# Optimization experiments

Measured on AMD Instinct MI355X. Metric: run time of the kernel, lower is better.

The kernel has to match this reference:

```python
import jax, jax.numpy as jnp
import numpy as np

DIM = 1024
N_HEADS = 16
HEAD_DIM = DIM // N_HEADS


def setup_inputs() -> dict:
    key = jax.random.key(0)
    k1, k2, k3 = jax.random.split(key, 3)
    x = jax.random.normal(k1, (1, 4096, DIM), dtype=jnp.float32)
    # nn.Linear weights stored as [out, in]; y = x @ W.T
    w_qkv = jax.random.normal(k2, (3 * DIM, DIM), dtype=jnp.float32) * (DIM ** -0.5)
    w_o = jax.random.normal(k3, (DIM, DIM), dtype=jnp.float32) * (DIM ** -0.5)
    return {"x": x, "w_qkv": w_qkv, "w_o": w_o}


def reference(x, w_qkv, w_o):
    b, s, _ = x.shape
    qkv = jnp.einsum('bsd,ed->bse', x, w_qkv)  # [b, s, 3*dim]
    qkv = qkv.reshape(b, s, 3, N_HEADS, HEAD_DIM)
    qkv = jnp.transpose(qkv, (2, 0, 3, 1, 4))  # [3, b, h, s, hd]
    q, k, v = qkv[0], qkv[1], qkv[2]
    scale = HEAD_DIM ** -0.5
    scores = jnp.einsum('bhqd,bhkd->bhqk', q, k) * scale  # full O(N^2) scores
    attn = jax.nn.softmax(scores, axis=-1)
    out = jnp.einsum('bhqk,bhkd->bhqd', attn, v)
    out = jnp.transpose(out, (0, 2, 1, 3)).reshape(b, s, DIM)
    return jnp.einsum('bsd,ed->bse', out, w_o)
```

## Files before the change

### kernel.cpp

```cpp
#include <hip/hip_runtime.h>

typedef __bf16 bf16x8 __attribute__((ext_vector_type(8)));
typedef float f32x4 __attribute__((ext_vector_type(4)));
typedef unsigned short ushort_t;
typedef unsigned int uint_t;

constexpr int S = 4096, DMODEL = 1024, NH = 16, HD = 64;
#define QSCALE 0.18033688011112042f

#if __has_builtin(__builtin_amdgcn_exp2f)
#define EXP2(x) __builtin_amdgcn_exp2f(x)
#else
#define EXP2(x) exp2f(x)
#endif

__device__ inline ushort_t f2bf(float f) {
  uint_t u = __builtin_bit_cast(uint_t, f);
  u = u + 0x7FFFu + ((u >> 16) & 1u);
  return (ushort_t)(u >> 16);
}

__device__ inline ushort_t f2bf_hw(float f) {
  __bf16 h = (__bf16)f;
  return __builtin_bit_cast(ushort_t, h);
}

__device__ inline void gl2lds16(const ushort_t* g, ushort_t* l) {
  __builtin_amdgcn_global_load_lds(
      (const __attribute__((address_space(1))) unsigned int*)g,
      (__attribute__((address_space(3))) unsigned int*)l, 16, 0, 0);
}

__global__ __launch_bounds__(256) void cvt_f32_bf16(const float* __restrict__ in,
                                                    ushort_t* __restrict__ out, int n4) {
  int i = blockIdx.x * 256 + threadIdx.x;
  if (i >= n4) return;
  float4 f = reinterpret_cast<const float4*>(in)[i];
  ushort4 o;
  o.x = f2bf(f.x); o.y = f2bf(f.y); o.z = f2bf(f.z); o.w = f2bf(f.w);
  reinterpret_cast<ushort4*>(out)[i] = o;
}

template <int EPI>
__global__ __launch_bounds__(256) void gemm_bt(const ushort_t* __restrict__ A,
                                               const ushort_t* __restrict__ B,
                                               int M, int N, int K,
                                               float* __restrict__ Cf,
                                               ushort_t* __restrict__ qb,
                                               ushort_t* __restrict__ kb,
                                               ushort_t* __restrict__ vtb) {
  __shared__ ushort_t sA[128 * 64];
  __shared__ ushort_t sB[128 * 64];
  const int t = threadIdx.x;
  const int lane = t & 63, w = t >> 6;
  const int wr = w >> 1, wc = w & 1;
  const int rA0 = blockIdx.y * 128, rB0 = blockIdx.x * 128;

  f32x4 acc[4][4];
#pragma unroll
  for (int m = 0; m < 4; ++m)
#pragma unroll
    for (int n = 0; n < 4; ++n) acc[m][n] = (f32x4){0.f, 0.f, 0.f, 0.f};

  const int srow = t >> 3;
  const int scol = (t & 7) * 8;
  const int ldsbase = w * 512;

  for (int k0 = 0; k0 < K; k0 += 64) {
#pragma unroll
    for (int i = 0; i < 4; ++i) {
      int r = i * 32 + srow;
      int kc = scol ^ ((r & 7) << 3);
      gl2lds16(&A[(size_t)(rA0 + r) * K + k0 + kc], &sA[i * 2048 + ldsbase]);
    }
#pragma unroll
    for (int i = 0; i < 4; ++i) {
      int r = i * 32 + srow;
      int kc = scol ^ ((r & 7) << 3);
      gl2lds16(&B[(size_t)(rB0 + r) * K + k0 + kc], &sB[i * 2048 + ldsbase]);
    }
    __syncthreads();
#pragma unroll
    for (int ks = 0; ks < 2; ++ks) {
      const int kk = ks * 32 + (lane >> 4) * 8;
      bf16x8 af[4], bfr[4];
#pragma unroll
      for (int m = 0; m < 4; ++m) {
        int row = wr * 64 + m * 16 + (lane & 15);
        af[m] = *(const bf16x8*)&sA[row * 64 + (kk ^ ((row & 7) << 3))];
      }
#pragma unroll
      for (int n = 0; n < 4; ++n) {
        int row = wc * 64 + n * 16 + (lane & 15);
        bfr[n] = *(const bf16x8*)&sB[row * 64 + (kk ^ ((row & 7) << 3))];
      }
#pragma unroll
      for (int m = 0; m < 4; ++m)
#pragma unroll
        for (int n = 0; n < 4; ++n)
          acc[m][n] = __builtin_amdgcn_mfma_f32_16x16x32_bf16(af[m], bfr[n], acc[m][n], 0, 0, 0);
    }
    __syncthreads();
  }

#pragma unroll
  for (int m = 0; m < 4; ++m)
#pragma unroll
    for (int n = 0; n < 4; ++n)
#pragma unroll
      for (int r = 0; r < 4; ++r) {
        int row = rA0 + wr * 64 + m * 16 + (lane >> 4) * 4 + r;
        int col = rB0 + wc * 64 + n * 16 + (lane & 15);
        float v = acc[m][n][r];
        if constexpr (EPI == 0) {
          Cf[(size_t)row * N + col] = v;
        } else {
          int t3 = col >> 10, h = (col >> 6) & 15, d = col & 63;
          if (t3 == 0)      qb[((size_t)h * S + row) * HD + d] = f2bf_hw(v * QSCALE);
          else if (t3 == 1) kb[((size_t)h * S + row) * HD + d] = f2bf_hw(v);
          else              vtb[((size_t)h * HD + d) * S + row] = f2bf_hw(v);
        }
      }
}

__global__ __launch_bounds__(256) void gemm_bt_n64(const ushort_t* __restrict__ A,
                                                   const ushort_t* __restrict__ B,
                                                   int M, int N, int K,
                                                   float* __restrict__ Cf) {
  __shared__ ushort_t sA[128 * 64];
  __shared__ ushort_t sB[64 * 64];
  const int t = threadIdx.x;
  const int lane = t & 63, w = t >> 6;
  const int wr = w >> 1, wc = w & 1;
  const int rA0 = blockIdx.y * 128, rB0 = blockIdx.x * 64;

  f32x4 acc[4][2];
#pragma unroll
  for (int m = 0; m < 4; ++m)
#pragma unroll
    for (int n = 0; n < 2; ++n) acc[m][n] = (f32x4){0.f, 0.f, 0.f, 0.f};

  const int srow = t >> 3;
  const int scol = (t & 7) * 8;
  const int ldsbase = w * 512;

  for (int k0 = 0; k0 < K; k0 += 64) {
#pragma unroll
    for (int i = 0; i < 4; ++i) {
      int r = i * 32 + srow;
      int kc = scol ^ ((r & 7) << 3);
      gl2lds16(&A[(size_t)(rA0 + r) * K + k0 + kc], &sA[i * 2048 + ldsbase]);
    }
#pragma unroll
    for (int i = 0; i < 2; ++i) {
      int r = i * 32 + srow;
      int kc = scol ^ ((r & 7) << 3);
      gl2lds16(&B[(size_t)(rB0 + r) * K + k0 + kc], &sB[i * 2048 + ldsbase]);
    }
    __syncthreads();
#pragma unroll
    for (int ks = 0; ks < 2; ++ks) {
      const int kk = ks * 32 + (lane >> 4) * 8;
      bf16x8 af[4], bfr[2];
#pragma unroll
      for (int m = 0; m < 4; ++m) {
        int row = wr * 64 + m * 16 + (lane & 15);
        af[m] = *(const bf16x8*)&sA[row * 64 + (kk ^ ((row & 7) << 3))];
      }
#pragma unroll
      for (int n = 0; n < 2; ++n) {
        int row = wc * 32 + n * 16 + (lane & 15);
        bfr[n] = *(const bf16x8*)&sB[row * 64 + (kk ^ ((row & 7) << 3))];
      }
#pragma unroll
      for (int m = 0; m < 4; ++m)
#pragma unroll
        for (int n = 0; n < 2; ++n)
          acc[m][n] = __builtin_amdgcn_mfma_f32_16x16x32_bf16(af[m], bfr[n], acc[m][n], 0, 0, 0);
    }
    __syncthreads();
  }

#pragma unroll
  for (int m = 0; m < 4; ++m)
#pragma unroll
    for (int n = 0; n < 2; ++n)
#pragma unroll
      for (int r = 0; r < 4; ++r) {
        int row = rA0 + wr * 64 + m * 16 + (lane >> 4) * 4 + r;
        int col = rB0 + wc * 32 + n * 16 + (lane & 15);
        Cf[(size_t)row * N + col] = acc[m][n][r];
      }
}

__global__ __launch_bounds__(512) void attn_fwd(const ushort_t* __restrict__ qb,
                                                const ushort_t* __restrict__ kb,
                                                const ushort_t* __restrict__ vtb,
                                                ushort_t* __restrict__ aob) {
  __shared__ ushort_t sK[3][64 * 64];
  __shared__ ushort_t sV[3][64 * 64];
  __shared__ ushort_t sP[8][16 * 64];
  const int t = threadIdx.x, lane = t & 63, w = t >> 6;
  const int f = blockIdx.x;
  const int sidx = (f & 7) * 64 + (f >> 3);
  const int h = sidx >> 5;
  const int q0 = (sidx & 31) * 128;
  const ushort_t* qh = qb + (size_t)h * S * HD;
  const ushort_t* kh = kb + (size_t)h * S * HD;
  const ushort_t* vh = vtb + (size_t)h * HD * S;

  bf16x8 qf[2];
  {
    int qr = q0 + w * 16 + (lane & 15);
    const ushort_t* p = &qh[(size_t)qr * HD + (lane >> 4) * 8];
    qf[0] = *(const bf16x8*)p;
    qf[1] = *(const bf16x8*)(p + 32);
  }
  f32x4 acc[4];
#pragma unroll
  for (int n = 0; n < 4; ++n) acc[n] = (f32x4){0.f, 0.f, 0.f, 0.f};
  float lsum[4] = {0.f, 0.f, 0.f, 0.f};

  const int srow = t >> 3;
  const int scol = (t & 7) * 8;
  const int kc = scol ^ ((srow & 7) << 3);
  const int ldsbase = w * 512;
  const int kk0 = (lane >> 4) * 8;

  auto stage = [&](int buf, int kv0) {
    gl2lds16(&kh[(size_t)(kv0 + srow) * HD + kc], &sK[buf][ldsbase]);
    gl2lds16(&vh[(size_t)srow * S + kv0 + kc], &sV[buf][ldsbase]);
  };

  constexpr int NT = S / 64;
  stage(0, 0);
  stage(1, 64);

  for (int ti = 0; ti < NT; ++ti) {
    const int buf = ti % 3;
    if (ti + 2 < NT) {
      stage((ti + 2) % 3, (ti + 2) * 64);
      asm volatile("s_waitcnt vmcnt(4)" ::: "memory");
    } else if (ti + 1 < NT) {
      asm volatile("s_waitcnt vmcnt(2)" ::: "memory");
    } else {
      asm volatile("s_waitcnt vmcnt(0)" ::: "memory");
    }
    __builtin_amdgcn_sched_barrier(0);
    __builtin_amdgcn_s_barrier();

    const ushort_t* Kb = &sK[buf][0];
    const ushort_t* Vb = &sV[buf][0];

    f32x4 sc[4];
    __builtin_amdgcn_s_setprio(1);
#pragma unroll
    for (int nt = 0; nt < 4; ++nt) {
      sc[nt] = (f32x4){0.f, 0.f, 0.f, 0.f};
      int row = nt * 16 + (lane & 15);
#pragma unroll
      for (int ks = 0; ks < 2; ++ks) {
        int kk = ks * 32 + kk0;
        bf16x8 kf = *(const bf16x8*)&Kb[row * 64 + (kk ^ ((row & 7) << 3))];
        sc[nt] = __builtin_amdgcn_mfma_f32_16x16x32_bf16(qf[ks], kf, sc[nt], 0, 0, 0);
      }
    }
    __builtin_amdgcn_s_setprio(0);

    float p[4][4];
#pragma unroll
    for (int r = 0; r < 4; ++r) {
      float ps = 0.f;
#pragma unroll
      for (int nt = 0; nt < 4; ++nt) {
        float pv = EXP2(sc[nt][r]);
        p[nt][r] = pv;
        ps += pv;
      }
      lsum[r] += ps;
    }
    const int prow_base = (lane >> 4) * 4;
#pragma unroll
    for (int nt = 0; nt < 4; ++nt) {
      int col = nt * 16 + (lane & 15);
#pragma unroll
      for (int r = 0; r < 4; ++r) {
        int row = prow_base + r;
        sP[w][row * 64 + (col ^ ((row & 7) << 3))] = f2bf_hw(p[nt][r]);
      }
    }
    bf16x8 pf[2];
    {
      int row = lane & 15;
#pragma unroll
      for (int ks = 0; ks < 2; ++ks) {
        int kk = ks * 32 + kk0;
        pf[ks] = *(const bf16x8*)&sP[w][row * 64 + (kk ^ ((row & 7) << 3))];
      }
    }
    __builtin_amdgcn_s_setprio(1);
#pragma unroll
    for (int nt = 0; nt < 4; ++nt) {
      int row = nt * 16 + (lane & 15);
#pragma unroll
      for (int ks = 0; ks < 2; ++ks) {
        int kk = ks * 32 + kk0;
        bf16x8 vf = *(const bf16x8*)&Vb[row * 64 + (kk ^ ((row & 7) << 3))];
        acc[nt] = __builtin_amdgcn_mfma_f32_16x16x32_bf16(pf[ks], vf, acc[nt], 0, 0, 0);
      }
    }
    __builtin_amdgcn_s_setprio(0);
    __builtin_amdgcn_s_barrier();
  }
  float linv[4];
#pragma unroll
  for (int r = 0; r < 4; ++r) {
    float l = lsum[r];
    l += __shfl_xor(l, 1);
    l += __shfl_xor(l, 2);
    l += __shfl_xor(l, 4);
    l += __shfl_xor(l, 8);
    linv[r] = 1.0f / l;
  }
#pragma unroll
  for (int nt = 0; nt < 4; ++nt)
#pragma unroll
    for (int r = 0; r < 4; ++r) {
      int row = q0 + w * 16 + (lane >> 4) * 4 + r;
      int col = h * HD + nt * 16 + (lane & 15);
      aob[(size_t)row * DMODEL + col] = f2bf_hw(acc[nt][r] * linv[r]);
    }
}

extern "C" void kernel_launch(void* const* d_in, const int* in_sizes, int n_in,
                              void* d_out, int out_size, void* d_ws, size_t ws_size,
                              hipStream_t stream) {
  const float* x = (const float*)d_in[0];
  const float* wqkv = (const float*)d_in[1];
  const float* wo = (const float*)d_in[2];
  float* out = (float*)d_out;
  char* ws = (char*)d_ws;
  const size_t MB = 1024ull * 1024ull;
  ushort_t* xb  = (ushort_t*)(ws);
  ushort_t* wqb = (ushort_t*)(ws + 8 * MB);
  ushort_t* wob = (ushort_t*)(ws + 14 * MB);
  ushort_t* qb  = (ushort_t*)(ws + 16 * MB);
  ushort_t* kb  = (ushort_t*)(ws + 24 * MB);
  ushort_t* vtb = (ushort_t*)(ws + 32 * MB);
  ushort_t* aob = (ushort_t*)(ws + 40 * MB);

  cvt_f32_bf16<<<(S * DMODEL / 4 + 255) / 256, 256, 0, stream>>>(x, xb, S * DMODEL / 4);
  cvt_f32_bf16<<<(3 * DMODEL * DMODEL / 4 + 255) / 256, 256, 0, stream>>>(wqkv, wqb, 3 * DMODEL * DMODEL / 4);
  cvt_f32_bf16<<<(DMODEL * DMODEL / 4 + 255) / 256, 256, 0, stream>>>(wo, wob, DMODEL * DMODEL / 4);

  dim3 g1(3 * DMODEL / 128, S / 128);
  gemm_bt<1><<<g1, 256, 0, stream>>>(xb, wqb, S, 3 * DMODEL, DMODEL, nullptr, qb, kb, vtb);

  attn_fwd<<<dim3(512), 512, 0, stream>>>(qb, kb, vtb, aob);

  dim3 g2(DMODEL / 64, S / 128);
  gemm_bt_n64<<<g2, 256, 0, stream>>>(aob, wob, S, DMODEL, DMODEL, out);
}
```

Before: 173.9 us.

## Give each attention wave two 16-row query tiles, halving waves per block

```diff
diff --git a/kernel.cpp b/kernel.cpp
--- a/kernel.cpp
+++ b/kernel.cpp
@@ -193,13 +193,13 @@
       }
 }
 
-__global__ __launch_bounds__(512) void attn_fwd(const ushort_t* __restrict__ qb,
+__global__ __launch_bounds__(256) void attn_fwd(const ushort_t* __restrict__ qb,
                                                 const ushort_t* __restrict__ kb,
                                                 const ushort_t* __restrict__ vtb,
                                                 ushort_t* __restrict__ aob) {
   __shared__ ushort_t sK[3][64 * 64];
   __shared__ ushort_t sV[3][64 * 64];
-  __shared__ ushort_t sP[8][16 * 64];
+  __shared__ ushort_t sP[4][32 * 64];
   const int t = threadIdx.x, lane = t & 63, w = t >> 6;
   const int f = blockIdx.x;
   const int sidx = (f & 7) * 64 + (f >> 3);
@@ -209,27 +209,39 @@
   const ushort_t* kh = kb + (size_t)h * S * HD;
   const ushort_t* vh = vtb + (size_t)h * HD * S;
 
-  bf16x8 qf[2];
-  {
-    int qr = q0 + w * 16 + (lane & 15);
-    const ushort_t* p = &qh[(size_t)qr * HD + (lane >> 4) * 8];
-    qf[0] = *(const bf16x8*)p;
-    qf[1] = *(const bf16x8*)(p + 32);
-  }
-  f32x4 acc[4];
-#pragma unroll
-  for (int n = 0; n < 4; ++n) acc[n] = (f32x4){0.f, 0.f, 0.f, 0.f};
-  float lsum[4] = {0.f, 0.f, 0.f, 0.f};
+  const int l15 = lane & 15, g = lane >> 4;
+  const int kk0 = g * 8;
+
+  bf16x8 qf[2][2];
+#pragma unroll
+  for (int qg = 0; qg < 2; ++qg) {
+    const ushort_t* p = &qh[(size_t)(q0 + w * 32 + qg * 16 + l15) * HD + kk0];
+    qf[qg][0] = *(const bf16x8*)p;
+    qf[qg][1] = *(const bf16x8*)(p + 32);
+  }
+  f32x4 acc[2][4];
+#pragma unroll
+  for (int qg = 0; qg < 2; ++qg)
+#pragma unroll
+    for (int n = 0; n < 4; ++n) acc[qg][n] = (f32x4){0.f, 0.f, 0.f, 0.f};
+  float lsum[2][4] = {{0.f, 0.f, 0.f, 0.f}, {0.f, 0.f, 0.f, 0.f}};
 
   const int srow = t >> 3;
   const int scol = (t & 7) * 8;
   const int kc = scol ^ ((srow & 7) << 3);
   const int ldsbase = w * 512;
-  const int kk0 = (lane >> 4) * 8;
 
   auto stage = [&](int buf, int kv0) {
-    gl2lds16(&kh[(size_t)(kv0 + srow) * HD + kc], &sK[buf][ldsbase]);
-    gl2lds16(&vh[(size_t)srow * S + kv0 + kc], &sV[buf][ldsbase]);
+#pragma unroll
+    for (int i = 0; i < 2; ++i) {
+      int r = i * 32 + srow;
+      gl2lds16(&kh[(size_t)(kv0 + r) * HD + kc], &sK[buf][i * 2048 + ldsbase]);
+    }
+#pragma unroll
+    for (int i = 0; i < 2; ++i) {
+      int r = i * 32 + srow;
+      gl2lds16(&vh[(size_t)r * S + kv0 + kc], &sV[buf][i * 2048 + ldsbase]);
+    }
   };
 
   constexpr int NT = S / 64;
@@ -240,9 +252,9 @@
     const int buf = ti % 3;
     if (ti + 2 < NT) {
       stage((ti + 2) % 3, (ti + 2) * 64);
+      asm volatile("s_waitcnt vmcnt(8)" ::: "memory");
+    } else if (ti + 1 < NT) {
       asm volatile("s_waitcnt vmcnt(4)" ::: "memory");
-    } else if (ti + 1 < NT) {
-      asm volatile("s_waitcnt vmcnt(2)" ::: "memory");
     } else {
       asm volatile("s_waitcnt vmcnt(0)" ::: "memory");
     }
@@ -252,84 +264,94 @@
     const ushort_t* Kb = &sK[buf][0];
     const ushort_t* Vb = &sV[buf][0];
 
-    f32x4 sc[4];
+    f32x4 sc[2][4];
     __builtin_amdgcn_s_setprio(1);
 #pragma unroll
     for (int nt = 0; nt < 4; ++nt) {
-      sc[nt] = (f32x4){0.f, 0.f, 0.f, 0.f};
-      int row = nt * 16 + (lane & 15);
-#pragma unroll
-      for (int ks = 0; ks < 2; ++ks) {
-        int kk = ks * 32 + kk0;
-        bf16x8 kf = *(const bf16x8*)&Kb[row * 64 + (kk ^ ((row & 7) << 3))];
-        sc[nt] = __builtin_amdgcn_mfma_f32_16x16x32_bf16(qf[ks], kf, sc[nt], 0, 0, 0);
+      int row = nt * 16 + l15;
+      const int rsw = (row & 7) << 3;
+      bf16x8 kf0 = *(const bf16x8*)&Kb[row * 64 + ((0 * 32 + kk0) ^ rsw)];
+      bf16x8 kf1 = *(const bf16x8*)&Kb[row * 64 + ((1 * 32 + kk0) ^ rsw)];
+#pragma unroll
+      for (int qg = 0; qg < 2; ++qg) {
+        sc[qg][nt] = __builtin_amdgcn_mfma_f32_16x16x32_bf16(qf[qg][0], kf0,
+                       (f32x4){0.f, 0.f, 0.f, 0.f}, 0, 0, 0);
+        sc[qg][nt] = __builtin_amdgcn_mfma_f32_16x16x32_bf16(qf[qg][1], kf1, sc[qg][nt], 0, 0, 0);
       }
     }
     __builtin_amdgcn_s_setprio(0);
 
-    float p[4][4];
-#pragma unroll
-    for (int r = 0; r < 4; ++r) {
-      float ps = 0.f;
+#pragma unroll
+    for (int qg = 0; qg < 2; ++qg)
+#pragma unroll
+      for (int r = 0; r < 4; ++r) {
+        float ps = 0.f;
+#pragma unroll
+        for (int nt = 0; nt < 4; ++nt) {
+          float pv = EXP2(sc[qg][nt][r]);
+          sc[qg][nt][r] = pv;
+          ps += pv;
+        }
+        lsum[qg][r] += ps;
+      }
+    const int prow_base = g * 4;
+#pragma unroll
+    for (int qg = 0; qg < 2; ++qg)
 #pragma unroll
       for (int nt = 0; nt < 4; ++nt) {
-        float pv = EXP2(sc[nt][r]);
-        p[nt][r] = pv;
-        ps += pv;
-      }
-      lsum[r] += ps;
-    }
-    const int prow_base = (lane >> 4) * 4;
+        int col = nt * 16 + l15;
+#pragma unroll
+        for (int r = 0; r < 4; ++r) {
+          int row = qg * 16 + prow_base + r;
+          sP[w][row * 64 + (col ^ ((row & 7) << 3))] = f2bf_hw(sc[qg][nt][r]);
+        }
+      }
+    bf16x8 pf[2][2];
+#pragma unroll
+    for (int qg = 0; qg < 2; ++qg) {
+      int row = qg * 16 + l15;
+      const int rsw = (row & 7) << 3;
+#pragma unroll
+      for (int ks = 0; ks < 2; ++ks)
+        pf[qg][ks] = *(const bf16x8*)&sP[w][row * 64 + ((ks * 32 + kk0) ^ rsw)];
+    }
+    __builtin_amdgcn_s_setprio(1);
 #pragma unroll
     for (int nt = 0; nt < 4; ++nt) {
-      int col = nt * 16 + (lane & 15);
-#pragma unroll
-      for (int r = 0; r < 4; ++r) {
-        int row = prow_base + r;
-        sP[w][row * 64 + (col ^ ((row & 7) << 3))] = f2bf_hw(p[nt][r]);
-      }
-    }
-    bf16x8 pf[2];
-    {
-      int row = lane & 15;
-#pragma unroll
-      for (int ks = 0; ks < 2; ++ks) {
-        int kk = ks * 32 + kk0;
-        pf[ks] = *(const bf16x8*)&sP[w][row * 64 + (kk ^ ((row & 7) << 3))];
-      }
-    }
-    __builtin_amdgcn_s_setprio(1);
-#pragma unroll
-    for (int nt = 0; nt < 4; ++nt) {
-      int row = nt * 16 + (lane & 15);
-#pragma unroll
-      for (int ks = 0; ks < 2; ++ks) {
-        int kk = ks * 32 + kk0;
-        bf16x8 vf = *(const bf16x8*)&Vb[row * 64 + (kk ^ ((row & 7) << 3))];
-        acc[nt] = __builtin_amdgcn_mfma_f32_16x16x32_bf16(pf[ks], vf, acc[nt], 0, 0, 0);
+      int row = nt * 16 + l15;
+      const int rsw = (row & 7) << 3;
+      bf16x8 vf0 = *(const bf16x8*)&Vb[row * 64 + ((0 * 32 + kk0) ^ rsw)];
+      bf16x8 vf1 = *(const bf16x8*)&Vb[row * 64 + ((1 * 32 + kk0) ^ rsw)];
+#pragma unroll
+      for (int qg = 0; qg < 2; ++qg) {
+        acc[qg][nt] = __builtin_amdgcn_mfma_f32_16x16x32_bf16(pf[qg][0], vf0, acc[qg][nt], 0, 0, 0);
+        acc[qg][nt] = __builtin_amdgcn_mfma_f32_16x16x32_bf16(pf[qg][1], vf1, acc[qg][nt], 0, 0, 0);
       }
     }
     __builtin_amdgcn_s_setprio(0);
     __builtin_amdgcn_s_barrier();
   }
-  float linv[4];
-#pragma unroll
-  for (int r = 0; r < 4; ++r) {
-    float l = lsum[r];
-    l += __shfl_xor(l, 1);
-    l += __shfl_xor(l, 2);
-    l += __shfl_xor(l, 4);
-    l += __shfl_xor(l, 8);
-    linv[r] = 1.0f / l;
-  }
-#pragma unroll
-  for (int nt = 0; nt < 4; ++nt)
+#pragma unroll
+  for (int qg = 0; qg < 2; ++qg) {
+    float linv[4];
 #pragma unroll
     for (int r = 0; r < 4; ++r) {
-      int row = q0 + w * 16 + (lane >> 4) * 4 + r;
-      int col = h * HD + nt * 16 + (lane & 15);
-      aob[(size_t)row * DMODEL + col] = f2bf_hw(acc[nt][r] * linv[r]);
-    }
+      float l = lsum[qg][r];
+      l += __shfl_xor(l, 1);
+      l += __shfl_xor(l, 2);
+      l += __shfl_xor(l, 4);
+      l += __shfl_xor(l, 8);
+      linv[r] = 1.0f / l;
+    }
+#pragma unroll
+    for (int nt = 0; nt < 4; ++nt)
+#pragma unroll
+      for (int r = 0; r < 4; ++r) {
+        int row = q0 + w * 32 + qg * 16 + g * 4 + r;
+        int col = h * HD + nt * 16 + l15;
+        aob[(size_t)row * DMODEL + col] = f2bf_hw(acc[qg][nt][r] * linv[r]);
+      }
+  }
 }
 
 extern "C" void kernel_launch(void* const* d_in, const int* in_sizes, int n_in,
@@ -356,7 +378,7 @@
   dim3 g1(3 * DMODEL / 128, S / 128);
   gemm_bt<1><<<g1, 256, 0, stream>>>(xb, wqb, S, 3 * DMODEL, DMODEL, nullptr, qb, kb, vtb);
 
-  attn_fwd<<<dim3(512), 512, 0, stream>>>(qb, kb, vtb, aob);
+  attn_fwd<<<dim3(512), 256, 0, stream>>>(qb, kb, vtb, aob);
 
   dim3 g2(DMODEL / 64, S / 128);
   gemm_bt_n64<<<g2, 256, 0, stream>>>(aob, wob, S, DMODEL, DMODEL, out);
```

New measurement: 190.6 us. 9.6% more time.
